# Performance work log

Measured on AMD Instinct MI355X. Metric: run time of the kernel, lower is better.

The kernel has to match this reference:

```python
import jax, jax.numpy as jnp
import numpy as np

N_NODES = 50000
N_EDGES = 800000
D_IN = 256
DIM_H = 256
N_GRAPHS = 500
N_OUT = 10
BN_EPS = 1e-5


def _mlp(h, W1, b1, gamma, beta, mean, var, W2, b2):
    # Linear -> BatchNorm1d (eval, running stats) -> ReLU -> Linear -> ReLU
    h = h @ W1 + b1
    h = (h - mean) * (gamma / jnp.sqrt(var + BN_EPS)) + beta
    h = jax.nn.relu(h)
    return jax.nn.relu(h @ W2 + b2)


def _gin_conv(x, src, dst, params):
    # PyG GINConv with eps=0: out = nn(x + sum_{j in N(i)} x_j)
    agg = jax.ops.segment_sum(x[src], dst, num_segments=N_NODES)
    return _mlp(x + agg, *params)


def setup_inputs() -> dict:
    key = jax.random.key(0)
    ks = jax.random.split(key, 24)
    x = jax.random.normal(ks[0], (N_NODES, D_IN), dtype=jnp.float32)
    edge_index = jax.random.randint(ks[1], (2, N_EDGES), 0, N_NODES, dtype=jnp.int64)
    batch = jnp.sort(jax.random.randint(ks[2], (N_NODES,), 0, N_GRAPHS, dtype=jnp.int64))

    def lin(k, fan_in, fan_out):
        s = 1.0 / np.sqrt(fan_in)
        kw, kb = jax.random.split(k)
        W = jax.random.uniform(kw, (fan_in, fan_out), minval=-s, maxval=s, dtype=jnp.float32)
        b = jax.random.uniform(kb, (fan_out,), minval=-s, maxval=s, dtype=jnp.float32)
        return W, b

    def bn(k, d):
        k1, k2, k3, k4 = jax.random.split(k, 4)
        gamma = 1.0 + 0.1 * jax.random.normal(k1, (d,), dtype=jnp.float32)
        beta = 0.1 * jax.random.normal(k2, (d,), dtype=jnp.float32)
        mean = 0.1 * jax.random.normal(k3, (d,), dtype=jnp.float32)
        var = jax.random.uniform(k4, (d,), minval=0.5, maxval=1.5, dtype=jnp.float32)
        return gamma, beta, mean, var

    W1a, b1a = lin(ks[3], D_IN, DIM_H)
    g1a, be1a, m1a, v1a = bn(ks[4], DIM_H)
    W2a, b2a = lin(ks[5], DIM_H, DIM_H)
    W1b, b1b = lin(ks[6], DIM_H, DIM_H)
    g1b, be1b, m1b, v1b = bn(ks[7], DIM_H)
    W2b, b2b = lin(ks[8], DIM_H, DIM_H)
    lin1_W, lin1_b = lin(ks[9], DIM_H * 2, DIM_H * 3)
    lin2_W, lin2_b = lin(ks[10], DIM_H * 3, N_OUT)

    return dict(x=x, edge_index=edge_index, batch=batch,
                W1a=W1a, b1a=b1a, g1a=g1a, be1a=be1a, m1a=m1a, v1a=v1a, W2a=W2a, b2a=b2a,
                W1b=W1b, b1b=b1b, g1b=g1b, be1b=be1b, m1b=m1b, v1b=v1b, W2b=W2b, b2b=b2b,
                lin1_W=lin1_W, lin1_b=lin1_b, lin2_W=lin2_W, lin2_b=lin2_b)


def reference(x, edge_index, batch,
              W1a, b1a, g1a, be1a, m1a, v1a, W2a, b2a,
              W1b, b1b, g1b, be1b, m1b, v1b, W2b, b2b,
              lin1_W, lin1_b, lin2_W, lin2_b):
    src, dst = edge_index[0], edge_index[1]
    h1 = _gin_conv(x, src, dst, (W1a, b1a, g1a, be1a, m1a, v1a, W2a, b2a))
    h2 = _gin_conv(h1, src, dst, (W1b, b1b, g1b, be1b, m1b, v1b, W2b, b2b))
    p1 = jax.ops.segment_sum(h1, batch, num_segments=N_GRAPHS)  # global_add_pool
    p2 = jax.ops.segment_sum(h2, batch, num_segments=N_GRAPHS)
    h = jnp.concatenate([p1, p2], axis=1)
    h = jax.nn.relu(h @ lin1_W + lin1_b)
    # dropout p=0.6 is identity in eval mode
    h = h @ lin2_W + lin2_b
    return jax.nn.log_softmax(h, axis=1)
```

## Files before the change

kernel.cpp:

```cpp
#include <hip/hip_runtime.h>

#define N_NODES 50000
#define MPAD 50176
#define N_EDGES 800000
#define DIM 256
#define N_GRAPHS 500
#define N_OUT 10
#define BN_EPS 1e-5f
#define SCAN_BS 1024
#define KSPLIT 4
#define SORT_CAP 96

typedef unsigned int u32;
typedef short bf16x8 __attribute__((ext_vector_type(8)));
typedef unsigned short us8 __attribute__((ext_vector_type(8)));
typedef float f32x4 __attribute__((ext_vector_type(4)));

typedef __attribute__((address_space(1))) const unsigned int gas_u32;
typedef __attribute__((address_space(3))) unsigned int las_u32;

__device__ inline void g2l16(const void* g, void* l) {
    __builtin_amdgcn_global_load_lds((gas_u32*)g, (las_u32*)l, 16, 0, 0);
}

__device__ inline float b2f(unsigned short u) {
    union { u32 i; float f; } c; c.i = ((u32)u) << 16; return c.f;
}
__device__ inline unsigned short f2b(float f) {
    u32 x = __builtin_bit_cast(u32, f);
    return (unsigned short)((x + 0x7FFFu + ((x >> 16) & 1u)) >> 16);
}

__device__ inline int mid_addr(int row, int col) {
    return row * 512 + ((((col >> 3) ^ (row & 31)) << 4) | ((col & 7) << 1));
}

__global__ void zero_i(int* __restrict__ p, int n) {
    int i = blockIdx.x * blockDim.x + threadIdx.x;
    if (i < n) p[i] = 0;
}
__global__ void hist_dst(const int* __restrict__ dst, int* __restrict__ deg) {
    int e = blockIdx.x * blockDim.x + threadIdx.x;
    if (e < N_EDGES) atomicAdd(&deg[dst[e]], 1);
}
__global__ void scan_phase1(const int* __restrict__ deg, int* __restrict__ rowptr,
                            int* __restrict__ bsum, int n) {
    __shared__ int sh[SCAN_BS];
    int i = blockIdx.x * SCAN_BS + threadIdx.x;
    int v = (i < n) ? deg[i] : 0;
    sh[threadIdx.x] = v;
    __syncthreads();
    for (int off = 1; off < SCAN_BS; off <<= 1) {
        int t = (threadIdx.x >= off) ? sh[threadIdx.x - off] : 0;
        __syncthreads();
        sh[threadIdx.x] += t;
        __syncthreads();
    }
    if (i < n) rowptr[i] = sh[threadIdx.x] - v;
    if (threadIdx.x == SCAN_BS - 1) bsum[blockIdx.x] = sh[threadIdx.x];
}
__global__ void scan_phase2(int* __restrict__ bsum, int nb) {
    if (threadIdx.x == 0 && blockIdx.x == 0) {
        int run = 0;
        for (int b = 0; b < nb; b++) { int v = bsum[b]; bsum[b] = run; run += v; }
    }
}
__global__ void scan_phase3(int* __restrict__ rowptr, int* __restrict__ cursor,
                            const int* __restrict__ bsum, int n) {
    int i = blockIdx.x * SCAN_BS + threadIdx.x;
    if (i < n) {
        int v = rowptr[i] + bsum[blockIdx.x];
        rowptr[i] = v;
        cursor[i] = v;
    }
    if (i == 0) rowptr[n] = N_EDGES;
}
__global__ void fill_csr(const int* __restrict__ src, const int* __restrict__ dst,
                         int* __restrict__ cursor, int* __restrict__ col) {
    int e = blockIdx.x * blockDim.x + threadIdx.x;
    if (e < N_EDGES) {
        int p = atomicAdd(&cursor[dst[e]], 1);
        col[p] = src[e];
    }
}
__global__ void sort_csr(const int* __restrict__ rowptr, int* __restrict__ col) {
    __shared__ int buf[4][SORT_CAP];
    int node = blockIdx.x * 4 + (threadIdx.x >> 6);
    if (node >= N_NODES) return;
    int lane = threadIdx.x & 63;
    int w = threadIdx.x >> 6;
    int s = rowptr[node], e = rowptr[node + 1];
    int L = e - s;
    if (L <= 1 || L > SORT_CAP) return;
    for (int i = lane; i < L; i += 64) buf[w][i] = col[s + i];
    asm volatile("s_waitcnt lgkmcnt(0) vmcnt(0)" ::: "memory");
    for (int pass = 0; pass < L; pass++) {
        int base = 2 * lane + (pass & 1);
        if (base + 1 < L) {
            int a = buf[w][base], b = buf[w][base + 1];
            if (a > b) { buf[w][base] = b; buf[w][base + 1] = a; }
        }
        asm volatile("s_waitcnt lgkmcnt(0)" ::: "memory");
    }
    for (int i = lane; i < L; i += 64) col[s + i] = buf[w][i];
}
__global__ void graph_starts(const int* __restrict__ batch, int* __restrict__ gstart) {
    int g = blockIdx.x * blockDim.x + threadIdx.x;
    if (g > N_GRAPHS) return;
    if (g == N_GRAPHS) { gstart[g] = N_NODES; return; }
    int lo = 0, hi = N_NODES;
    while (lo < hi) { int mid = (lo + hi) >> 1; if (batch[mid] < g) lo = mid + 1; else hi = mid; }
    gstart[g] = lo;
}

__global__ void conv_x(const float4* __restrict__ in, ushort4* __restrict__ out, int n4) {
    int i = blockIdx.x * blockDim.x + threadIdx.x;
    if (i < n4) {
        float4 v = in[i];
        ushort4 o; o.x = f2b(v.x); o.y = f2b(v.y); o.z = f2b(v.z); o.w = f2b(v.w);
        out[i] = o;
    }
}
__global__ void conv_wt4(const float* __restrict__ W0, const float* __restrict__ W1,
                         const float* __restrict__ W2, const float* __restrict__ W3,
                         unsigned short* __restrict__ Wt) {
    int mat = blockIdx.y;
    const float* W = (mat == 0) ? W0 : (mat == 1) ? W1 : (mat == 2) ? W2 : W3;
    int n = blockIdx.x;
    int k = threadIdx.x;
    Wt[((size_t)mat << 16) + (size_t)n * 256 + k] = f2b(W[(size_t)k * 256 + n]);
}
__global__ void make_ss(const float* __restrict__ bias, const float* __restrict__ gamma,
                        const float* __restrict__ beta, const float* __restrict__ mean,
                        const float* __restrict__ var, float* __restrict__ scale,
                        float* __restrict__ shift) {
    int i = threadIdx.x;
    float s = gamma[i] * rsqrtf(var[i] + BN_EPS);
    scale[i] = s;
    shift[i] = (bias[i] - mean[i]) * s + beta[i];
}

__global__ void gather_bf(const unsigned short* __restrict__ feat,
                          const int* __restrict__ col,
                          const int* __restrict__ rowptr,
                          unsigned short* __restrict__ out) {
    int node = blockIdx.x * 4 + (threadIdx.x >> 6);
    if (node >= N_NODES) return;
    int lane = threadIdx.x & 63;
    int half = lane >> 5;
    int d8 = (lane & 31) * 8;
    float acc[8];
    #pragma unroll
    for (int j = 0; j < 8; j++) acc[j] = 0.f;
    if (half == 0) {
        us8 own = *reinterpret_cast<const us8*>(&feat[(size_t)node * DIM + d8]);
        #pragma unroll
        for (int j = 0; j < 8; j++) acc[j] = b2f((unsigned short)own[j]);
    }
    int s = rowptr[node], e = rowptr[node + 1];
    int i = s + half;
    for (; i + 6 < e; i += 8) {
        int n0 = col[i], n1 = col[i + 2], n2 = col[i + 4], n3 = col[i + 6];
        us8 v0 = *reinterpret_cast<const us8*>(&feat[(size_t)n0 * DIM + d8]);
        us8 v1 = *reinterpret_cast<const us8*>(&feat[(size_t)n1 * DIM + d8]);
        us8 v2 = *reinterpret_cast<const us8*>(&feat[(size_t)n2 * DIM + d8]);
        us8 v3 = *reinterpret_cast<const us8*>(&feat[(size_t)n3 * DIM + d8]);
        #pragma unroll
        for (int j = 0; j < 8; j++)
            acc[j] += (b2f((unsigned short)v0[j]) + b2f((unsigned short)v1[j]))
                    + (b2f((unsigned short)v2[j]) + b2f((unsigned short)v3[j]));
    }
    for (; i < e; i += 2) {
        int n0 = col[i];
        us8 v0 = *reinterpret_cast<const us8*>(&feat[(size_t)n0 * DIM + d8]);
        #pragma unroll
        for (int j = 0; j < 8; j++) acc[j] += b2f((unsigned short)v0[j]);
    }
    #pragma unroll
    for (int j = 0; j < 8; j++) acc[j] += __shfl_xor(acc[j], 32, 64);
    if (half == 0) {
        us8 o;
        #pragma unroll
        for (int j = 0; j < 8; j++) o[j] = (short)f2b(acc[j]);
        *reinterpret_cast<us8*>(&out[(size_t)node * DIM + d8]) = o;
    }
}

__global__ __launch_bounds__(256, 2)
void fused_mlp(const unsigned short* __restrict__ A,
               const unsigned short* __restrict__ W1t,
               const unsigned short* __restrict__ W2t,
               const float* __restrict__ scale1,
               const float* __restrict__ shift1,
               const float* __restrict__ shift2,
               unsigned short* __restrict__ H, int M) {
    __shared__ __align__(16) unsigned short Asb[64 * 64];
    __shared__ __align__(16) unsigned short Bsb[256 * 64];
    __shared__ __align__(16) unsigned short midb[64 * 256];

    int t = threadIdx.x;
    int wave = t >> 6, lane = t & 63;
    int m0 = blockIdx.x * 64;
    int wc = wave * 64;
    int rsel = lane & 15;
    int kgrp = lane >> 4;
    int cr = lane >> 4;

    float s1[4], sh1[4], sh2[4];
    #pragma unroll
    for (int n = 0; n < 4; n++) {
        int colg = wc + n * 16 + rsel;
        s1[n]  = scale1[colg];
        sh1[n] = shift1[colg];
        sh2[n] = shift2[colg];
    }

    f32x4 acc[4][4];
    #pragma unroll
    for (int m = 0; m < 4; m++)
        #pragma unroll
        for (int n = 0; n < 4; n++)
            acc[m][n] = (f32x4){0.f, 0.f, 0.f, 0.f};

    int arow0 = t >> 3, achk0 = t & 7;
    int arow1 = (256 + t) >> 3, achk1 = t & 7;
    const char* Abase = (const char*)A + (size_t)m0 * 512;

    for (int ks = 0; ks < 4; ks++) {
        size_t ko = (size_t)ks * 128;
        g2l16(Abase + (size_t)arow0 * 512 + ko + ((achk0 ^ (arow0 & 7)) << 4),
              (char*)Asb + (size_t)t * 16);
        g2l16(Abase + (size_t)arow1 * 512 + ko + ((achk1 ^ (arow1 & 7)) << 4),
              (char*)Asb + (size_t)(256 + t) * 16);
        #pragma unroll
        for (int i = 0; i < 8; i++) {
            int s = i * 256 + t;
            int brow = s >> 3, bchk = s & 7;
            g2l16((const char*)W1t + (size_t)brow * 512 + ko + ((bchk ^ (brow & 7)) << 4),
                  (char*)Bsb + (size_t)s * 16);
        }
        __syncthreads();

        #pragma unroll
        for (int ksub = 0; ksub < 2; ksub++) {
            bf16x8 af[4], bfr[4];
            int kchunk = ksub * 4 + kgrp;
            #pragma unroll
            for (int m = 0; m < 4; m++) {
                int row = m * 16 + rsel;
                af[m] = *(const bf16x8*)((const char*)Asb + (size_t)row * 128
                                         + ((kchunk ^ (row & 7)) << 4));
            }
            #pragma unroll
            for (int n = 0; n < 4; n++) {
                int row = wc + n * 16 + rsel;
                bfr[n] = *(const bf16x8*)((const char*)Bsb + (size_t)row * 128
                                          + ((kchunk ^ (row & 7)) << 4));
            }
            #pragma unroll
            for (int m = 0; m < 4; m++)
                #pragma unroll
                for (int n = 0; n < 4; n++)
                    acc[m][n] = __builtin_amdgcn_mfma_f32_16x16x32_bf16(af[m], bfr[n], acc[m][n], 0, 0, 0);
        }
        __syncthreads();
    }

    #pragma unroll
    for (int n = 0; n < 4; n++) {
        int colg = wc + n * 16 + rsel;
        #pragma unroll
        for (int m = 0; m < 4; m++) {
            int rowb = m * 16 + cr * 4;
            #pragma unroll
            for (int r = 0; r < 4; r++) {
                float v = fmaxf(acc[m][n][r] * s1[n] + sh1[n], 0.f);
                *(unsigned short*)((char*)midb + mid_addr(rowb + r, colg)) = f2b(v);
                acc[m][n][r] = 0.f;
            }
        }
    }

    for (int ks = 0; ks < 4; ks++) {
        size_t ko = (size_t)ks * 128;
        #pragma unroll
        for (int i = 0; i < 8; i++) {
            int s = i * 256 + t;
            int brow = s >> 3, bchk = s & 7;
            g2l16((const char*)W2t + (size_t)brow * 512 + ko + ((bchk ^ (brow & 7)) << 4),
                  (char*)Bsb + (size_t)s * 16);
        }
        __syncthreads();

        #pragma unroll
        for (int ksub = 0; ksub < 2; ksub++) {
            bf16x8 af[4], bfr[4];
            int kchunk = ksub * 4 + kgrp;
            int kcol = ks * 64 + ksub * 32 + kgrp * 8;
            #pragma unroll
            for (int m = 0; m < 4; m++)
                af[m] = *(const bf16x8*)((const char*)midb + mid_addr(m * 16 + rsel, kcol));
            #pragma unroll
            for (int n = 0; n < 4; n++) {
                int row = wc + n * 16 + rsel;
                bfr[n] = *(const bf16x8*)((const char*)Bsb + (size_t)row * 128
                                          + ((kchunk ^ (row & 7)) << 4));
            }
            #pragma unroll
            for (int m = 0; m < 4; m++)
                #pragma unroll
                for (int n = 0; n < 4; n++)
                    acc[m][n] = __builtin_amdgcn_mfma_f32_16x16x32_bf16(af[m], bfr[n], acc[m][n], 0, 0, 0);
        }
        __syncthreads();
    }

    #pragma unroll
    for (int n = 0; n < 4; n++) {
        int colg = wc + n * 16 + rsel;
        #pragma unroll
        for (int m = 0; m < 4; m++) {
            int rowb = m0 + m * 16 + cr * 4;
            #pragma unroll
            for (int r = 0; r < 4; r++) {
                int row = rowb + r;
                if (row < M) {
                    float v = fmaxf(acc[m][n][r] + sh2[n], 0.f);
                    H[(size_t)row * 256 + colg] = f2b(v);
                }
            }
        }
    }
}

__global__ void pool_seg(const unsigned short* __restrict__ h1,
                         const unsigned short* __restrict__ h2,
                         const int* __restrict__ gstart,
                         float* __restrict__ pcat) {
    __shared__ float red1[8][256];
    __shared__ float red2[8][256];
    int g = blockIdx.x;
    int t = threadIdx.x;
    int sub = t >> 5;
    int d8 = (t & 31) * 8;
    float a1[8], a2[8];
    #pragma unroll
    for (int j = 0; j < 8; j++) { a1[j] = 0.f; a2[j] = 0.f; }
    int s = gstart[g], e = gstart[g + 1];
    for (int n = s + sub; n < e; n += 8) {
        us8 v1 = *reinterpret_cast<const us8*>(&h1[(size_t)n * DIM + d8]);
        us8 v2 = *reinterpret_cast<const us8*>(&h2[(size_t)n * DIM + d8]);
        #pragma unroll
        for (int j = 0; j < 8; j++) {
            a1[j] += b2f((unsigned short)v1[j]);
            a2[j] += b2f((unsigned short)v2[j]);
        }
    }
    #pragma unroll
    for (int j = 0; j < 8; j++) {
        red1[sub][d8 + j] = a1[j];
        red2[sub][d8 + j] = a2[j];
    }
    __syncthreads();
    float o1 = 0.f, o2 = 0.f;
    #pragma unroll
    for (int k = 0; k < 8; k++) { o1 += red1[k][t]; o2 += red2[k][t]; }
    pcat[(size_t)g * 512 + t]       = o1;
    pcat[(size_t)g * 512 + 256 + t] = o2;
}

__global__ void head1(const float* __restrict__ A,
                      const float* __restrict__ W1,
                      float* __restrict__ Hpart) {
    __shared__ float As[16][65];
    __shared__ float Bs[16][65];
    int t = threadIdx.x;
    int m0 = blockIdx.y * 64;
    int n0 = blockIdx.x * 64;
    int kz = blockIdx.z * (512 / KSPLIT);
    int tx = t & 15, ty = t >> 4;
    float acc[4][4] = {};
    for (int k0 = kz; k0 < kz + 512 / KSPLIT; k0 += 16) {
        #pragma unroll
        for (int i = 0; i < 4; i++) {
            int r = (t >> 4) + i * 16;
            int k = t & 15;
            int gr = m0 + r;
            As[k][r] = (gr < N_GRAPHS) ? A[(size_t)gr * 512 + k0 + k] : 0.f;
        }
        #pragma unroll
        for (int i = 0; i < 4; i++) {
            int k = (t >> 6) + i * 4;
            int n = t & 63;
            Bs[k][n] = W1[(size_t)(k0 + k) * 768 + n0 + n];
        }
        __syncthreads();
        #pragma unroll
        for (int k = 0; k < 16; k++) {
            float a[4], b[4];
            #pragma unroll
            for (int i = 0; i < 4; i++) a[i] = As[k][ty * 4 + i];
            #pragma unroll
            for (int j = 0; j < 4; j++) b[j] = Bs[k][tx * 4 + j];
            #pragma unroll
            for (int i = 0; i < 4; i++)
                #pragma unroll
                for (int j = 0; j < 4; j++)
                    acc[i][j] += a[i] * b[j];
        }
        __syncthreads();
    }
    float* Hz = Hpart + (size_t)blockIdx.z * N_GRAPHS * 768;
    #pragma unroll
    for (int i = 0; i < 4; i++) {
        int gm = m0 + ty * 4 + i;
        if (gm >= N_GRAPHS) continue;
        #pragma unroll
        for (int j = 0; j < 4; j++) {
            int gn = n0 + tx * 4 + j;
            Hz[(size_t)gm * 768 + gn] = acc[i][j];
        }
    }
}

__global__ void head2(const float* __restrict__ Hpart, const float* __restrict__ b1,
                      const float* __restrict__ W2, const float* __restrict__ b2,
                      float* __restrict__ out) {
    int g = blockIdx.x;
    int lane = threadIdx.x;
    float part[N_OUT];
    #pragma unroll
    for (int o = 0; o < N_OUT; o++) part[o] = 0.f;
    for (int k = lane; k < 768; k += 64) {
        float hv = b1[k];
        #pragma unroll
        for (int z = 0; z < KSPLIT; z++)
            hv += Hpart[((size_t)z * N_GRAPHS + g) * 768 + k];
        hv = fmaxf(hv, 0.f);
        #pragma unroll
        for (int o = 0; o < N_OUT; o++) part[o] += hv * W2[(size_t)k * N_OUT + o];
    }
    #pragma unroll
    for (int o = 0; o < N_OUT; o++) {
        #pragma unroll
        for (int off = 32; off > 0; off >>= 1)
            part[o] += __shfl_down(part[o], off, 64);
    }
    if (lane == 0) {
        float logits[N_OUT];
        float mx = -1e30f;
        #pragma unroll
        for (int o = 0; o < N_OUT; o++) { logits[o] = part[o] + b2[o]; mx = fmaxf(mx, logits[o]); }
        float ssum = 0.f;
        #pragma unroll
        for (int o = 0; o < N_OUT; o++) ssum += expf(logits[o] - mx);
        float lse = logf(ssum);
        #pragma unroll
        for (int o = 0; o < N_OUT; o++)
            out[(size_t)g * N_OUT + o] = logits[o] - mx - lse;
    }
}

extern "C" void kernel_launch(void* const* d_in, const int* in_sizes, int n_in,
                              void* d_out, int out_size, void* d_ws, size_t ws_size,
                              hipStream_t stream) {
    const float* x     = (const float*)d_in[0];
    const int*   ei    = (const int*)d_in[1];
    const int*   batch = (const int*)d_in[2];
    const float* W1a = (const float*)d_in[3];
    const float* b1a = (const float*)d_in[4];
    const float* g1a = (const float*)d_in[5];
    const float* be1a= (const float*)d_in[6];
    const float* m1a = (const float*)d_in[7];
    const float* v1a = (const float*)d_in[8];
    const float* W2a = (const float*)d_in[9];
    const float* b2a = (const float*)d_in[10];
    const float* W1b = (const float*)d_in[11];
    const float* b1b = (const float*)d_in[12];
    const float* g1b = (const float*)d_in[13];
    const float* be1b= (const float*)d_in[14];
    const float* m1b = (const float*)d_in[15];
    const float* v1b = (const float*)d_in[16];
    const float* W2b = (const float*)d_in[17];
    const float* b2b = (const float*)d_in[18];
    const float* lin1_W = (const float*)d_in[19];
    const float* lin1_b = (const float*)d_in[20];
    const float* lin2_W = (const float*)d_in[21];
    const float* lin2_b = (const float*)d_in[22];

    const size_t NBUF = (size_t)MPAD * DIM;
    char* ws = (char*)d_ws;
    unsigned short* agg  = (unsigned short*)ws;            ws += NBUF * 2;
    unsigned short* h1   = (unsigned short*)ws;            ws += NBUF * 2;
    unsigned short* h2   = (unsigned short*)ws;            ws += NBUF * 2;
    unsigned short* x_bf = (unsigned short*)ws;            ws += (size_t)N_NODES * DIM * 2;
    unsigned short* Wt   = (unsigned short*)ws;            ws += 4 * 65536 * 2;
    float* ss    = (float*)ws;                             ws += 4 * 256 * 4;
    float* pcat  = (float*)ws;                             ws += (size_t)N_GRAPHS * 512 * 4;
    float* Hpart = (float*)ws;                             ws += (size_t)KSPLIT * N_GRAPHS * 768 * 4;
    int* deg     = (int*)ws;                               ws += (size_t)N_NODES * 4;
    int* cursor  = (int*)ws;                               ws += (size_t)N_NODES * 4;
    int* rowptr  = (int*)ws;                               ws += (size_t)(N_NODES + 1) * 4;
    int* bsum    = (int*)ws;                               ws += 64 * 4;
    int* col     = (int*)ws;                               ws += (size_t)N_EDGES * 4;
    int* gstart  = (int*)ws;

    const int* srcE = ei;
    const int* dstE = ei + N_EDGES;

    const int nscan = (N_NODES + SCAN_BS - 1) / SCAN_BS;

    zero_i<<<(N_NODES + 255) / 256, 256, 0, stream>>>(deg, N_NODES);
    hist_dst<<<(N_EDGES + 255) / 256, 256, 0, stream>>>(dstE, deg);
    scan_phase1<<<nscan, SCAN_BS, 0, stream>>>(deg, rowptr, bsum, N_NODES);
    scan_phase2<<<1, 64, 0, stream>>>(bsum, nscan);
    scan_phase3<<<nscan, SCAN_BS, 0, stream>>>(rowptr, cursor, bsum, N_NODES);
    fill_csr<<<(N_EDGES + 255) / 256, 256, 0, stream>>>(srcE, dstE, cursor, col);
    sort_csr<<<(N_NODES + 3) / 4, 256, 0, stream>>>(rowptr, col);
    graph_starts<<<2, 256, 0, stream>>>(batch, gstart);

    conv_x<<<(N_NODES * DIM / 4 + 255) / 256, 256, 0, stream>>>(
        (const float4*)x, (ushort4*)x_bf, N_NODES * DIM / 4);
    dim3 wt_grid(256, 4);
    conv_wt4<<<wt_grid, 256, 0, stream>>>(W1a, W2a, W1b, W2b, Wt);
    make_ss<<<1, 256, 0, stream>>>(b1a, g1a, be1a, m1a, v1a, ss + 0 * 512, ss + 0 * 512 + 256);
    make_ss<<<1, 256, 0, stream>>>(b1b, g1b, be1b, m1b, v1b, ss + 1 * 512, ss + 1 * 512 + 256);

    gather_bf<<<(N_NODES + 3) / 4, 256, 0, stream>>>(x_bf, col, rowptr, agg);
    fused_mlp<<<MPAD / 64, 256, 0, stream>>>(agg, Wt + 0 * 65536, Wt + 1 * 65536,
                                             ss + 0 * 512, ss + 0 * 512 + 256, b2a, h1, N_NODES);

    gather_bf<<<(N_NODES + 3) / 4, 256, 0, stream>>>(h1, col, rowptr, agg);
    fused_mlp<<<MPAD / 64, 256, 0, stream>>>(agg, Wt + 2 * 65536, Wt + 3 * 65536,
                                             ss + 1 * 512, ss + 1 * 512 + 256, b2b, h2, N_NODES);

    pool_seg<<<N_GRAPHS, 256, 0, stream>>>(h1, h2, gstart, pcat);
    dim3 h1grid(12, 8, KSPLIT);
    head1<<<h1grid, 256, 0, stream>>>(pcat, lin1_W, Hpart);
    head2<<<N_GRAPHS, 64, 0, stream>>>(Hpart, lin1_b, lin2_W, lin2_b, (float*)d_out);
}
```

Before: 361.4 us.

## Replace fp32 split-K head GEMM with bf16 MFMA kernel fusing bias and ReLU

The pooled features are now stored as bf16, and lin1_W is converted to a transposed bf16 layout by a new conversion kernel. The head's first linear layer then runs as a bf16 MFMA GEMM with swizzled LDS tiles, and bias plus ReLU are applied in its epilogue. This drops the four-way split-K partial buffers and the reduction that head2 used to do. It adds an extra conversion launch and lowers the precision of the head computation. The grid shrinks to 24 blocks, so parallelism is limited, although this stage is small overall.

```diff
diff --git a/kernel.cpp b/kernel.cpp
--- a/kernel.cpp
+++ b/kernel.cpp
@@ -5,10 +5,10 @@
 #define N_EDGES 800000
 #define DIM 256
 #define N_GRAPHS 500
+#define GPAD 512
 #define N_OUT 10
 #define BN_EPS 1e-5f
 #define SCAN_BS 1024
-#define KSPLIT 4
 #define SORT_CAP 96
 
 typedef unsigned int u32;
@@ -130,6 +130,12 @@
     int k = threadIdx.x;
     Wt[((size_t)mat << 16) + (size_t)n * 256 + k] = f2b(W[(size_t)k * 256 + n]);
 }
+__global__ void conv_w1h(const float* __restrict__ W, unsigned short* __restrict__ Wh) {
+    int n = blockIdx.x;
+    int k = threadIdx.x;
+    Wh[(size_t)n * 512 + k]       = f2b(W[(size_t)k * 768 + n]);
+    Wh[(size_t)n * 512 + 256 + k] = f2b(W[(size_t)(256 + k) * 768 + n]);
+}
 __global__ void make_ss(const float* __restrict__ bias, const float* __restrict__ gamma,
                         const float* __restrict__ beta, const float* __restrict__ mean,
                         const float* __restrict__ var, float* __restrict__ scale,
@@ -336,7 +342,7 @@
 __global__ void pool_seg(const unsigned short* __restrict__ h1,
                          const unsigned short* __restrict__ h2,
                          const int* __restrict__ gstart,
-                         float* __restrict__ pcat) {
+                         unsigned short* __restrict__ pcat) {
     __shared__ float red1[8][256];
     __shared__ float red2[8][256];
     int g = blockIdx.x;
@@ -365,78 +371,107 @@
     float o1 = 0.f, o2 = 0.f;
     #pragma unroll
     for (int k = 0; k < 8; k++) { o1 += red1[k][t]; o2 += red2[k][t]; }
-    pcat[(size_t)g * 512 + t]       = o1;
-    pcat[(size_t)g * 512 + 256 + t] = o2;
-}
-
-__global__ void head1(const float* __restrict__ A,
-                      const float* __restrict__ W1,
-                      float* __restrict__ Hpart) {
-    __shared__ float As[16][65];
-    __shared__ float Bs[16][65];
+    pcat[(size_t)g * 512 + t]       = f2b(o1);
+    pcat[(size_t)g * 512 + 256 + t] = f2b(o2);
+}
+
+__global__ __launch_bounds__(256)
+void head1_mfma(const unsigned short* __restrict__ A,
+                const unsigned short* __restrict__ Wh,
+                const float* __restrict__ b1,
+                float* __restrict__ Hf) {
+    __shared__ __align__(16) unsigned short Asb[64 * 64];
+    __shared__ __align__(16) unsigned short Bsb[256 * 64];
+
     int t = threadIdx.x;
+    int wave = t >> 6, lane = t & 63;
+    int n0 = blockIdx.x * 256;
     int m0 = blockIdx.y * 64;
-    int n0 = blockIdx.x * 64;
-    int kz = blockIdx.z * (512 / KSPLIT);
-    int tx = t & 15, ty = t >> 4;
-    float acc[4][4] = {};
-    for (int k0 = kz; k0 < kz + 512 / KSPLIT; k0 += 16) {
-        #pragma unroll
-        for (int i = 0; i < 4; i++) {
-            int r = (t >> 4) + i * 16;
-            int k = t & 15;
-            int gr = m0 + r;
-            As[k][r] = (gr < N_GRAPHS) ? A[(size_t)gr * 512 + k0 + k] : 0.f;
-        }
-        #pragma unroll
-        for (int i = 0; i < 4; i++) {
-            int k = (t >> 6) + i * 4;
-            int n = t & 63;
-            Bs[k][n] = W1[(size_t)(k0 + k) * 768 + n0 + n];
-        }
-        __syncthreads();
-        #pragma unroll
-        for (int k = 0; k < 16; k++) {
-            float a[4], b[4];
-            #pragma unroll
-            for (int i = 0; i < 4; i++) a[i] = As[k][ty * 4 + i];
-            #pragma unroll
-            for (int j = 0; j < 4; j++) b[j] = Bs[k][tx * 4 + j];
-            #pragma unroll
-            for (int i = 0; i < 4; i++)
+    int wc = wave * 64;
+    int rsel = lane & 15;
+    int kgrp = lane >> 4;
+    int cr = lane >> 4;
+
+    float bb[4];
+    #pragma unroll
+    for (int n = 0; n < 4; n++) bb[n] = b1[n0 + wc + n * 16 + rsel];
+
+    f32x4 acc[4][4];
+    #pragma unroll
+    for (int m = 0; m < 4; m++)
+        #pragma unroll
+        for (int n = 0; n < 4; n++)
+            acc[m][n] = (f32x4){0.f, 0.f, 0.f, 0.f};
+
+    int arow0 = t >> 3, achk0 = t & 7;
+    int arow1 = (256 + t) >> 3, achk1 = t & 7;
+    const char* Abase = (const char*)A + (size_t)m0 * 1024;
+
+    for (int ks = 0; ks < 8; ks++) {
+        size_t ko = (size_t)ks * 128;
+        g2l16(Abase + (size_t)arow0 * 1024 + ko + ((achk0 ^ (arow0 & 7)) << 4),
+              (char*)Asb + (size_t)t * 16);
+        g2l16(Abase + (size_t)arow1 * 1024 + ko + ((achk1 ^ (arow1 & 7)) << 4),
+              (char*)Asb + (size_t)(256 + t) * 16);
+        #pragma unroll
+        for (int i = 0; i < 8; i++) {
+            int s = i * 256 + t;
+            int brow = s >> 3, bchk = s & 7;
+            g2l16((const char*)Wh + (size_t)(n0 + brow) * 1024 + ko + ((bchk ^ (brow & 7)) << 4),
+                  (char*)Bsb + (size_t)s * 16);
+        }
+        __syncthreads();
+
+        #pragma unroll
+        for (int ksub = 0; ksub < 2; ksub++) {
+            bf16x8 af[4], bfr[4];
+            int kchunk = ksub * 4 + kgrp;
+            #pragma unroll
+            for (int m = 0; m < 4; m++) {
+                int row = m * 16 + rsel;
+                af[m] = *(const bf16x8*)((const char*)Asb + (size_t)row * 128
+                                         + ((kchunk ^ (row & 7)) << 4));
+            }
+            #pragma unroll
+            for (int n = 0; n < 4; n++) {
+                int row = wc + n * 16 + rsel;
+                bfr[n] = *(const bf16x8*)((const char*)Bsb + (size_t)row * 128
+                                          + ((kchunk ^ (row & 7)) << 4));
+            }
+            #pragma unroll
+            for (int m = 0; m < 4; m++)
                 #pragma unroll
-                for (int j = 0; j < 4; j++)
-                    acc[i][j] += a[i] * b[j];
-        }
-        __syncthreads();
-    }
-    float* Hz = Hpart + (size_t)blockIdx.z * N_GRAPHS * 768;
-    #pragma unroll
-    for (int i = 0; i < 4; i++) {
-        int gm = m0 + ty * 4 + i;
-        if (gm >= N_GRAPHS) continue;
-        #pragma unroll
-        for (int j = 0; j < 4; j++) {
-            int gn = n0 + tx * 4 + j;
-            Hz[(size_t)gm * 768 + gn] = acc[i][j];
-        }
-    }
-}
-
-__global__ void head2(const float* __restrict__ Hpart, const float* __restrict__ b1,
-                      const float* __restrict__ W2, const float* __restrict__ b2,
-                      float* __restrict__ out) {
+                for (int n = 0; n < 4; n++)
+                    acc[m][n] = __builtin_amdgcn_mfma_f32_16x16x32_bf16(af[m], bfr[n], acc[m][n], 0, 0, 0);
+        }
+        __syncthreads();
+    }
+
+    #pragma unroll
+    for (int n = 0; n < 4; n++) {
+        int colg = n0 + wc + n * 16 + rsel;
+        #pragma unroll
+        for (int m = 0; m < 4; m++) {
+            int rowb = m0 + m * 16 + cr * 4;
+            #pragma unroll
+            for (int r = 0; r < 4; r++) {
+                int row = rowb + r;
+                if (row < N_GRAPHS)
+                    Hf[(size_t)row * 768 + colg] = fmaxf(acc[m][n][r] + bb[n], 0.f);
+            }
+        }
+    }
+}
+
+__global__ void head2(const float* __restrict__ Hf, const float* __restrict__ W2,
+                      const float* __restrict__ b2, float* __restrict__ out) {
     int g = blockIdx.x;
     int lane = threadIdx.x;
     float part[N_OUT];
     #pragma unroll
     for (int o = 0; o < N_OUT; o++) part[o] = 0.f;
     for (int k = lane; k < 768; k += 64) {
-        float hv = b1[k];
-        #pragma unroll
-        for (int z = 0; z < KSPLIT; z++)
-            hv += Hpart[((size_t)z * N_GRAPHS + g) * 768 + k];
-        hv = fmaxf(hv, 0.f);
+        float hv = Hf[(size_t)g * 768 + k];
         #pragma unroll
         for (int o = 0; o < N_OUT; o++) part[o] += hv * W2[(size_t)k * N_OUT + o];
     }
@@ -495,9 +530,10 @@
     unsigned short* h2   = (unsigned short*)ws;            ws += NBUF * 2;
     unsigned short* x_bf = (unsigned short*)ws;            ws += (size_t)N_NODES * DIM * 2;
     unsigned short* Wt   = (unsigned short*)ws;            ws += 4 * 65536 * 2;
+    unsigned short* W1h  = (unsigned short*)ws;            ws += (size_t)768 * 512 * 2;
     float* ss    = (float*)ws;                             ws += 4 * 256 * 4;
-    float* pcat  = (float*)ws;                             ws += (size_t)N_GRAPHS * 512 * 4;
-    float* Hpart = (float*)ws;                             ws += (size_t)KSPLIT * N_GRAPHS * 768 * 4;
+    unsigned short* pcat = (unsigned short*)ws;            ws += (size_t)GPAD * 512 * 2;
+    float* Hf    = (float*)ws;                             ws += (size_t)GPAD * 768 * 4;
     int* deg     = (int*)ws;                               ws += (size_t)N_NODES * 4;
     int* cursor  = (int*)ws;                               ws += (size_t)N_NODES * 4;
     int* rowptr  = (int*)ws;                               ws += (size_t)(N_NODES + 1) * 4;
@@ -523,6 +559,7 @@
         (const float4*)x, (ushort4*)x_bf, N_NODES * DIM / 4);
     dim3 wt_grid(256, 4);
     conv_wt4<<<wt_grid, 256, 0, stream>>>(W1a, W2a, W1b, W2b, Wt);
+    conv_w1h<<<768, 256, 0, stream>>>(lin1_W, W1h);
     make_ss<<<1, 256, 0, stream>>>(b1a, g1a, be1a, m1a, v1a, ss + 0 * 512, ss + 0 * 512 + 256);
     make_ss<<<1, 256, 0, stream>>>(b1b, g1b, be1b, m1b, v1b, ss + 1 * 512, ss + 1 * 512 + 256);
 
@@ -535,7 +572,7 @@
                                              ss + 1 * 512, ss + 1 * 512 + 256, b2b, h2, N_NODES);
 
     pool_seg<<<N_GRAPHS, 256, 0, stream>>>(h1, h2, gstart, pcat);
-    dim3 h1grid(12, 8, KSPLIT);
-    head1<<<h1grid, 256, 0, stream>>>(pcat, lin1_W, Hpart);
-    head2<<<N_GRAPHS, 64, 0, stream>>>(Hpart, lin1_b, lin2_W, lin2_b, (float*)d_out);
-}
+    dim3 h1grid(3, 8);
+    head1_mfma<<<h1grid, 256, 0, stream>>>(pcat, W1h, lin1_b, Hf);
+    head2<<<N_GRAPHS, 64, 0, stream>>>(Hf, lin2_W, lin2_b, (float*)d_out);
+}
```

After: 350.9 us. -2.9%, faster.
